# Kernel optimization log

Hardware: AMD Instinct MI355X
Metric: run time of the kernel (lower is better)

## Reference

```python
import jax, jax.numpy as jnp
import numpy as np

B, S, D, E, K = 4, 2048, 1024, 8, 2
DF = 4 * D


def setup_inputs() -> dict:
    key = jax.random.key(0)
    ks = jax.random.split(key, 7)
    x = jax.random.normal(ks[0], (B, S, D), dtype=jnp.float32)
    Wr = jax.random.normal(ks[1], (D, E), dtype=jnp.float32) * 0.02
    br = jnp.zeros((E,), dtype=jnp.float32)
    W1 = jax.random.normal(ks[2], (E, D, DF), dtype=jnp.float32) * 0.02
    b1 = jnp.zeros((E, DF), dtype=jnp.float32)
    W2 = jax.random.normal(ks[3], (E, DF, D), dtype=jnp.float32) * 0.02
    b2 = jnp.zeros((E, D), dtype=jnp.float32)
    return {"x": x, "Wr": Wr, "br": br, "W1": W1, "b1": b1, "W2": W2, "b2": b2}


def reference(x, Wr, br, W1, b1, W2, b2):
    # Router: softmax gates then top-k
    gates = jax.nn.softmax(x @ Wr + br, axis=-1)               # [B,S,E]
    topk_vals, topk_idx = jax.lax.top_k(gates, K)              # [B,S,K]

    # Per-(token, expert) combine weight: gate value if expert selected else 0
    onehot = jax.nn.one_hot(topk_idx, E, dtype=gates.dtype)    # [B,S,K,E]
    combine = jnp.sum(onehot * topk_vals[..., None], axis=2)   # [B,S,E]

    # Expert MLPs (loop over fixed small expert count, fully vectorized per expert)
    output = jnp.zeros_like(x)
    for e in range(E):
        h = jax.nn.gelu(x @ W1[e] + b1[e], approximate=False)  # [B,S,4D]
        y = h @ W2[e] + b2[e]                                  # [B,S,D]
        output = output + combine[..., e:e + 1] * y

    # Load-balancing aux loss (dispatch mask: 1.0 where expert selected)
    dispatch = jnp.max(onehot, axis=2)                         # [B,S,E]
    mean_gates = gates.mean(axis=(0, 1))
    mean_dispatch = dispatch.mean(axis=(0, 1))
    aux_loss = jnp.sum(mean_gates * mean_dispatch) * E / (B * S)
    return output, aux_loss
```

## Files before the change

### kernel.cpp

```cpp
#include <hip/hip_runtime.h>
#include <hip/hip_bf16.h>
#include <hip/hip_fp16.h>

typedef _Float16 f16;
typedef _Float16 half8 __attribute__((ext_vector_type(8)));
typedef _Float16 half4 __attribute__((ext_vector_type(4)));
typedef float   floatx4 __attribute__((ext_vector_type(4)));

#define N_TOK   8192
#define D_DIM   1024
#define E_NUM   8
#define DF_DIM  4096
#define MAX_SLOTS 17408
#define MAX_RT    136

#define MI_COUNT  0
#define MI_CURSOR 8
#define MI_OFF    16
#define MI_TOTAL  25
#define MI_RTE    26
#define MI_SUMG   168

__device__ __forceinline__ void gld_lds16(const void* g, void* l) {
    __builtin_amdgcn_global_load_lds(
        (__attribute__((address_space(1))) const void*)g,
        (__attribute__((address_space(3))) void*)l, 16, 0, 0);
}

__device__ __forceinline__ float gelu_f(float v) {
    float u = 0.7978845608028654f * v * (1.0f + 0.044715f * v * v);
    float t = __expf(-2.0f * fabsf(u));
    float th = (1.0f - t) / (1.0f + t);
    th = (u >= 0.f) ? th : -th;
    return 0.5f * v * (1.0f + th);
}

__global__ __launch_bounds__(256) void convert_x_kernel(
    const float* __restrict__ x, f16* __restrict__ xh)
{
    int idx = blockIdx.x * 256 + threadIdx.x;
    const int stride = gridDim.x * 256;
    const int n4 = (N_TOK * D_DIM) / 4;
    for (int i = idx; i < n4; i += stride) {
        float4 v = ((const float4*)x)[i];
        half4 o = { (f16)v.x, (f16)v.y, (f16)v.z, (f16)v.w };
        ((half4*)xh)[i] = o;
    }
}

__global__ __launch_bounds__(256) void transpose_conv_kernel(
    const float* __restrict__ src, f16* __restrict__ dst, int R, int C)
{
    const float* s = src + (size_t)blockIdx.z * R * C;
    f16* d = dst + (size_t)blockIdx.z * R * C;
    __shared__ float tile[64 * 65];
    const int rb = blockIdx.y * 64, cb = blockIdx.x * 64;
    const int tid = threadIdx.x;
#pragma unroll
    for (int j = 0; j < 4; ++j) {
        int lin = j * 1024 + tid * 4;
        int r = lin >> 6, c = lin & 63;
        float4 v = *(const float4*)(s + (size_t)(rb + r) * C + (cb + c));
        tile[r * 65 + c + 0] = v.x; tile[r * 65 + c + 1] = v.y;
        tile[r * 65 + c + 2] = v.z; tile[r * 65 + c + 3] = v.w;
    }
    __syncthreads();
#pragma unroll
    for (int j = 0; j < 4; ++j) {
        int lin = j * 1024 + tid * 4;
        int c = lin >> 6, r = lin & 63;
        half4 o = { (f16)tile[(r + 0) * 65 + c], (f16)tile[(r + 1) * 65 + c],
                    (f16)tile[(r + 2) * 65 + c], (f16)tile[(r + 3) * 65 + c] };
        *(half4*)(d + (size_t)(cb + c) * R + (rb + r)) = o;
    }
}

__global__ __launch_bounds__(256) void router_kernel(
    const float* __restrict__ x, const float* __restrict__ Wr,
    const float* __restrict__ br,
    int* __restrict__ topk_idx, float* __restrict__ topk_w,
    int* __restrict__ meta)
{
    const int w = threadIdx.x >> 6, l = threadIdx.x & 63;
    __shared__ float blk_sg[E_NUM];
    __shared__ int   blk_cnt[E_NUM];
    if (threadIdx.x < E_NUM) { blk_sg[threadIdx.x] = 0.f; blk_cnt[threadIdx.x] = 0; }
    __syncthreads();

    for (int it = 0; it < 4; ++it) {
        const int t = blockIdx.x * 16 + w * 4 + it;
        const float* xr = x + (size_t)t * D_DIM + l * 16;
        float acc[E_NUM] = {0.f,0.f,0.f,0.f,0.f,0.f,0.f,0.f};
#pragma unroll
        for (int i = 0; i < 16; i += 4) {
            float4 xv = *(const float4*)(xr + i);
            const float xs[4] = {xv.x, xv.y, xv.z, xv.w};
#pragma unroll
            for (int jj = 0; jj < 4; ++jj) {
                int d = l * 16 + i + jj;
                float4 w0 = *(const float4*)(Wr + (size_t)d * 8);
                float4 w1 = *(const float4*)(Wr + (size_t)d * 8 + 4);
                acc[0] += xs[jj] * w0.x; acc[1] += xs[jj] * w0.y;
                acc[2] += xs[jj] * w0.z; acc[3] += xs[jj] * w0.w;
                acc[4] += xs[jj] * w1.x; acc[5] += xs[jj] * w1.y;
                acc[6] += xs[jj] * w1.z; acc[7] += xs[jj] * w1.w;
            }
        }
#pragma unroll
        for (int e = 0; e < E_NUM; ++e) {
#pragma unroll
            for (int off = 32; off > 0; off >>= 1)
                acc[e] += __shfl_down(acc[e], off);
        }
        if (l == 0) {
            float lg[E_NUM], g[E_NUM];
            float mx = -1e30f;
#pragma unroll
            for (int e = 0; e < E_NUM; ++e) { lg[e] = acc[e] + br[e]; mx = fmaxf(mx, lg[e]); }
            float sum = 0.f;
#pragma unroll
            for (int e = 0; e < E_NUM; ++e) { g[e] = __expf(lg[e] - mx); sum += g[e]; }
            float inv = 1.f / sum;
#pragma unroll
            for (int e = 0; e < E_NUM; ++e) g[e] *= inv;
            int e1 = 0; float v1 = g[0];
#pragma unroll
            for (int e = 1; e < E_NUM; ++e) if (g[e] > v1) { v1 = g[e]; e1 = e; }
            int e2 = -1; float v2 = -1.f;
#pragma unroll
            for (int e = 0; e < E_NUM; ++e) if (e != e1 && g[e] > v2) { v2 = g[e]; e2 = e; }
            topk_idx[t * 2 + 0] = e1; topk_idx[t * 2 + 1] = e2;
            topk_w[t * 2 + 0] = v1;   topk_w[t * 2 + 1] = v2;
#pragma unroll
            for (int e = 0; e < E_NUM; ++e) atomicAdd(&blk_sg[e], g[e]);
            atomicAdd(&blk_cnt[e1], 1); atomicAdd(&blk_cnt[e2], 1);
        }
    }
    __syncthreads();
    if (threadIdx.x < E_NUM) {
        atomicAdd((float*)(meta + MI_SUMG) + threadIdx.x, blk_sg[threadIdx.x]);
        atomicAdd(meta + MI_COUNT + threadIdx.x, blk_cnt[threadIdx.x]);
    }
}

__global__ void scan_kernel(int* __restrict__ meta, float* __restrict__ out_aux)
{
    if (threadIdx.x != 0 || blockIdx.x != 0) return;
    int off = 0;
    for (int e = 0; e < E_NUM; ++e) {
        meta[MI_OFF + e] = off;
        int cnt = meta[MI_COUNT + e];
        int padded = ((cnt + 127) >> 7) << 7;
        for (int rt = off >> 7; rt < (off + padded) >> 7; ++rt)
            meta[MI_RTE + rt] = e;
        off += padded;
    }
    meta[MI_OFF + E_NUM] = off;
    meta[MI_TOTAL] = off >> 7;
    const float* sg = (const float*)(meta + MI_SUMG);
    float aux = 0.f;
    for (int e = 0; e < E_NUM; ++e)
        aux += (sg[e] / (float)N_TOK) * ((float)meta[MI_COUNT + e] / (float)N_TOK);
    out_aux[0] = aux * (float)E_NUM / (float)N_TOK;
}

__global__ __launch_bounds__(256) void fill_kernel(
    const int* __restrict__ topk_idx, const float* __restrict__ topk_w,
    int* __restrict__ meta, int* __restrict__ slot_token, float* __restrict__ slot_weight,
    int* __restrict__ slot_of)
{
    int t = blockIdx.x * 256 + threadIdx.x;
#pragma unroll
    for (int k = 0; k < 2; ++k) {
        int e = topk_idx[t * 2 + k];
        int p = atomicAdd(meta + MI_CURSOR + e, 1);
        int slot = meta[MI_OFF + e] + p;
        slot_token[slot] = t;
        slot_weight[slot] = topk_w[t * 2 + k];
        slot_of[t * 2 + k] = slot;
    }
}


#define STAGE_HALF(T, H) do {                                                  \
    f16* ld_ = smem + ((T)&1)*16384 + ((H)&1)*8192 + ((H)>>1)*4096;            \
    const f16* s_ = ((H)&1) ? bsrc[(H)>>1] : asrc[(H)>>1];                     \
    gld_lds16(s_ + (size_t)(T)*64, ld_ + tid*8);                               \
} while(0)

#define READ_AB() do {                                                         \
    _Pragma("unroll")                                                          \
    for (int mj = 0; mj < 4; ++mj) {                                           \
        const f16* pa_ = LA + (size_t)(rA + mj*16) * 64;                       \
        af[mj][0] = *(const half8*)(pa_ + sw0);                                \
        af[mj][1] = *(const half8*)(pa_ + sw1);                                \
    }                                                                          \
    _Pragma("unroll")                                                          \
    for (int nj = 0; nj < 2; ++nj) {                                           \
        const f16* pb_ = LB + (size_t)(rB + nj*16) * 64;                       \
        bf[nj][0] = *(const half8*)(pb_ + sw0);                                \
        bf[nj][1] = *(const half8*)(pb_ + sw1);                                \
    }                                                                          \
} while(0)

#define MFMA_MJ(MJ) do {                                                       \
    __builtin_amdgcn_s_setprio(1);                                             \
    _Pragma("unroll")                                                          \
    for (int nj = 0; nj < 2; ++nj) {                                           \
        acc[MJ][nj] = __builtin_amdgcn_mfma_f32_16x16x32_f16(                  \
            af[MJ][0], bf[nj][0], acc[MJ][nj], 0, 0, 0);                       \
        acc[MJ][nj] = __builtin_amdgcn_mfma_f32_16x16x32_f16(                  \
            af[MJ][1], bf[nj][1], acc[MJ][nj], 0, 0, 0);                       \
    }                                                                          \
    __builtin_amdgcn_s_setprio(0);                                             \
} while(0)

template<int KD, int NCOLS, int KSPLIT, bool GATHER, bool GELU, bool BIAS>
__global__ __launch_bounds__(512, 4) void gemm128_kernel(
    const f16* __restrict__ A, const f16* __restrict__ Bw,
    const float* __restrict__ bias, const int* __restrict__ slot_token,
    const int* __restrict__ meta, f16* __restrict__ Out, size_t out_kp_stride)
{
    constexpr int KLOC = KD / KSPLIT;
    constexpr int NT = KLOC / 64;
    __shared__ __align__(16) f16 smem[32768];

    const int rt = blockIdx.y;
    if (rt >= meta[MI_TOTAL]) return;
    const int e  = meta[MI_RTE + rt];
    const int nt = blockIdx.x;
    const int kp = blockIdx.z;
    const int kbase = kp * KLOC;

    const int tid = threadIdx.x;
    const int w = tid >> 6, l = tid & 63;
    const int wr2 = w >> 2, wc2 = w & 3;
    const int fr = l & 15, fq = l >> 4;

    const int srow = tid >> 3;
    const int kcs  = (tid & 7) ^ (srow & 7);

    const f16* asrc[2]; const f16* bsrc[2];
#pragma unroll
    for (int i = 0; i < 2; ++i) {
        int r = i * 64 + srow;
        int ar;
        if (GATHER) ar = slot_token[rt * 128 + r];
        else        ar = rt * 128 + r;
        asrc[i] = A + (size_t)ar * KD + kbase + kcs * 8;
        bsrc[i] = Bw + ((size_t)e * NCOLS + (size_t)nt * 128 + r) * KD + kbase + kcs * 8;
    }

    const int rA  = wr2 * 64 + fr;
    const int rB  = wc2 * 32 + fr;
    const int sw0 = ( fq      ^ (fr & 7)) * 8;
    const int sw1 = ((4 + fq) ^ (fr & 7)) * 8;

    floatx4 acc[4][2];
#pragma unroll
    for (int m = 0; m < 4; ++m)
#pragma unroll
        for (int n = 0; n < 2; ++n) acc[m][n] = (floatx4){0.f, 0.f, 0.f, 0.f};

    half8 af[4][2];
    half8 bf[2][2];

    STAGE_HALF(0, 0); STAGE_HALF(0, 1); STAGE_HALF(0, 2); STAGE_HALF(0, 3);
    STAGE_HALF(1, 0);
    asm volatile("s_waitcnt vmcnt(1)" ::: "memory");
    __builtin_amdgcn_s_barrier();

#pragma unroll 2
    for (int t = 0; t < NT; ++t) {
        const f16* LA = smem + (t & 1) * 16384;
        const f16* LB = LA + 8192;
        if (t + 1 < NT) { STAGE_HALF(t + 1, 1); STAGE_HALF(t + 1, 2); STAGE_HALF(t + 1, 3); }
        READ_AB();
        MFMA_MJ(0); MFMA_MJ(1); MFMA_MJ(2);
        asm volatile("s_waitcnt lgkmcnt(0)" ::: "memory");
        __builtin_amdgcn_s_barrier();
        if (t + 2 < NT) STAGE_HALF(t + 2, 0);
        MFMA_MJ(3);
        if (t + 1 < NT) {
            if (t + 1 < NT - 1) asm volatile("s_waitcnt vmcnt(1)" ::: "memory");
            else                asm volatile("s_waitcnt vmcnt(0)" ::: "memory");
            __builtin_amdgcn_s_barrier();
        }
    }

    f16* Op = Out + (size_t)kp * out_kp_stride;
    const int orow0 = rt * 128 + wr2 * 64;
    const int ocol0 = nt * 128 + wc2 * 32;
#pragma unroll
    for (int mj = 0; mj < 4; ++mj) {
#pragma unroll
        for (int nj = 0; nj < 2; ++nj) {
            const int col = ocol0 + nj * 16 + fr;
            float bs = 0.f;
            if (BIAS) bs = bias[(size_t)e * NCOLS + col];
#pragma unroll
            for (int j = 0; j < 4; ++j) {
                const int row = orow0 + mj * 16 + fq * 4 + j;
                float v = acc[mj][nj][j] + bs;
                if (GELU) v = gelu_f(v);
                Op[(size_t)row * NCOLS + col] = (f16)v;
            }
        }
    }
}

__global__ __launch_bounds__(256) void combine_kernel(
    const f16* __restrict__ P, const int* __restrict__ slot_of,
    const int* __restrict__ topk_idx, const float* __restrict__ topk_w,
    const float* __restrict__ b2, float* __restrict__ out)
{
    const int t = blockIdx.x;
    const int c = threadIdx.x;
    const size_t PS = (size_t)MAX_SLOTS * D_DIM;
    const int s0 = slot_of[t * 2], s1 = slot_of[t * 2 + 1];
    const int e0 = topk_idx[t * 2], e1 = topk_idx[t * 2 + 1];
    const float w0 = topk_w[t * 2], w1 = topk_w[t * 2 + 1];
    half4 a0 = *(const half4*)(P + (size_t)s0 * D_DIM + c * 4);
    half4 a1 = *(const half4*)(P + PS + (size_t)s0 * D_DIM + c * 4);
    half4 c0 = *(const half4*)(P + (size_t)s1 * D_DIM + c * 4);
    half4 c1 = *(const half4*)(P + PS + (size_t)s1 * D_DIM + c * 4);
    float4 bb0 = *(const float4*)(b2 + (size_t)e0 * D_DIM + c * 4);
    float4 bb1 = *(const float4*)(b2 + (size_t)e1 * D_DIM + c * 4);
    float4 o;
    o.x = w0 * ((float)a0[0] + (float)a1[0] + bb0.x) + w1 * ((float)c0[0] + (float)c1[0] + bb1.x);
    o.y = w0 * ((float)a0[1] + (float)a1[1] + bb0.y) + w1 * ((float)c0[1] + (float)c1[1] + bb1.y);
    o.z = w0 * ((float)a0[2] + (float)a1[2] + bb0.z) + w1 * ((float)c0[2] + (float)c1[2] + bb1.z);
    o.w = w0 * ((float)a0[3] + (float)a1[3] + bb0.w) + w1 * ((float)c0[3] + (float)c1[3] + bb1.w);
    *(float4*)(out + (size_t)t * D_DIM + c * 4) = o;
}

extern "C" void kernel_launch(void* const* d_in, const int* in_sizes, int n_in,
                              void* d_out, int out_size, void* d_ws, size_t ws_size,
                              hipStream_t stream) {
    const float* x  = (const float*)d_in[0];
    const float* Wr = (const float*)d_in[1];
    const float* br = (const float*)d_in[2];
    const float* W1 = (const float*)d_in[3];
    const float* b1 = (const float*)d_in[4];
    const float* W2 = (const float*)d_in[5];
    const float* b2 = (const float*)d_in[6];
    float* out = (float*)d_out;

    char* ws = (char*)d_ws;
    const size_t SZ_XH  = (size_t)N_TOK * D_DIM * 2;
    const size_t SZ_W1T = (size_t)E_NUM * DF_DIM * D_DIM * 2;
    const size_t SZ_W2T = SZ_W1T;
    const size_t SZ_H   = (size_t)MAX_SLOTS * DF_DIM * 2;

    f16* xh  = (f16*)(ws);
    f16* W1t = (f16*)(ws + SZ_XH);
    f16* W2t = (f16*)(ws + SZ_XH + SZ_W1T);
    f16* H   = (f16*)(ws + SZ_XH + SZ_W1T + SZ_W2T);
    f16* P   = (f16*)ws;
    char* p  = ws + SZ_XH + SZ_W1T + SZ_W2T + SZ_H;
    int*   topk_idx    = (int*)p;    p += (size_t)N_TOK * 2 * 4;
    float* topk_w      = (float*)p;  p += (size_t)N_TOK * 2 * 4;
    int*   slot_token  = (int*)p;    p += (size_t)MAX_SLOTS * 4;
    float* slot_weight = (float*)p;  p += (size_t)MAX_SLOTS * 4;
    int*   slot_of     = (int*)p;    p += (size_t)N_TOK * 2 * 4;
    int*   meta        = (int*)p;

    hipMemsetAsync(slot_token, 0, (size_t)MAX_SLOTS * 8 + (size_t)N_TOK * 2 * 4 + 1024, stream);

    convert_x_kernel<<<2048, 256, 0, stream>>>(x, xh);
    transpose_conv_kernel<<<dim3(DF_DIM / 64, D_DIM / 64, E_NUM), 256, 0, stream>>>(W1, W1t, D_DIM, DF_DIM);
    transpose_conv_kernel<<<dim3(D_DIM / 64, DF_DIM / 64, E_NUM), 256, 0, stream>>>(W2, W2t, DF_DIM, D_DIM);
    router_kernel<<<N_TOK / 16, 256, 0, stream>>>(x, Wr, br, topk_idx, topk_w, meta);
    scan_kernel<<<1, 64, 0, stream>>>(meta, out + (size_t)N_TOK * D_DIM);
    fill_kernel<<<N_TOK / 256, 256, 0, stream>>>(topk_idx, topk_w, meta, slot_token, slot_weight, slot_of);

    gemm128_kernel<D_DIM, DF_DIM, 1, true, true, true>
        <<<dim3(DF_DIM / 128, MAX_RT, 1), 512, 0, stream>>>(
        xh, W1t, b1, slot_token, meta, H, 0);

    gemm128_kernel<DF_DIM, D_DIM, 2, false, false, false>
        <<<dim3(D_DIM / 128, MAX_RT, 2), 512, 0, stream>>>(
        H, W2t, nullptr, slot_token, meta, P, (size_t)MAX_SLOTS * D_DIM);

    combine_kernel<<<N_TOK, 256, 0, stream>>>(P, slot_of, topk_idx, topk_w, b2, out);

    (void)in_sizes; (void)n_in; (void)ws_size;
}
```

Before: 635.7 us.

## Simplify GEMM to single-buffered 256-thread tiles with 64x64 per-wave output

Replaces the double-buffered, prefetching GEMM main loop with a single-buffered load-wait-compute loop using 256-thread blocks. Each wave now computes a 64x64 sub-tile with 16 accumulators, raising MFMA work per LDS read. The scan kernel fills the row-tile-to-expert table in parallel. In exchange, global-to-LDS loads no longer overlap with MFMA compute, and register pressure rises.

```diff
diff --git a/kernel.cpp b/kernel.cpp
--- a/kernel.cpp
+++ b/kernel.cpp
@@ -143,25 +143,35 @@
     }
 }
 
-__global__ void scan_kernel(int* __restrict__ meta, float* __restrict__ out_aux)
-{
-    if (threadIdx.x != 0 || blockIdx.x != 0) return;
-    int off = 0;
-    for (int e = 0; e < E_NUM; ++e) {
-        meta[MI_OFF + e] = off;
-        int cnt = meta[MI_COUNT + e];
-        int padded = ((cnt + 127) >> 7) << 7;
-        for (int rt = off >> 7; rt < (off + padded) >> 7; ++rt)
-            meta[MI_RTE + rt] = e;
-        off += padded;
-    }
-    meta[MI_OFF + E_NUM] = off;
-    meta[MI_TOTAL] = off >> 7;
-    const float* sg = (const float*)(meta + MI_SUMG);
-    float aux = 0.f;
-    for (int e = 0; e < E_NUM; ++e)
-        aux += (sg[e] / (float)N_TOK) * ((float)meta[MI_COUNT + e] / (float)N_TOK);
-    out_aux[0] = aux * (float)E_NUM / (float)N_TOK;
+__global__ __launch_bounds__(256) void scan_kernel(int* __restrict__ meta, float* __restrict__ out_aux)
+{
+    __shared__ int offs[E_NUM + 1];
+    const int tid = threadIdx.x;
+    if (tid == 0) {
+        int off = 0;
+        for (int e = 0; e < E_NUM; ++e) {
+            meta[MI_OFF + e] = off;
+            offs[e] = off;
+            int cnt = meta[MI_COUNT + e];
+            off += ((cnt + 127) >> 7) << 7;
+        }
+        meta[MI_OFF + E_NUM] = off;
+        offs[E_NUM] = off;
+        meta[MI_TOTAL] = off >> 7;
+        const float* sg = (const float*)(meta + MI_SUMG);
+        float aux = 0.f;
+        for (int e = 0; e < E_NUM; ++e)
+            aux += (sg[e] / (float)N_TOK) * ((float)meta[MI_COUNT + e] / (float)N_TOK);
+        out_aux[0] = aux * (float)E_NUM / (float)N_TOK;
+    }
+    __syncthreads();
+    const int total = offs[E_NUM] >> 7;
+    for (int rt = tid; rt < total; rt += 256) {
+        int row = rt << 7, e = 0;
+#pragma unroll
+        for (int k = 1; k < E_NUM; ++k) if (row >= offs[k]) e = k;
+        meta[MI_RTE + rt] = e;
+    }
 }
 
 __global__ __launch_bounds__(256) void fill_kernel(
@@ -182,48 +192,16 @@
 }
 
 
-#define STAGE_HALF(T, H) do {                                                  \
-    f16* ld_ = smem + ((T)&1)*16384 + ((H)&1)*8192 + ((H)>>1)*4096;            \
-    const f16* s_ = ((H)&1) ? bsrc[(H)>>1] : asrc[(H)>>1];                     \
-    gld_lds16(s_ + (size_t)(T)*64, ld_ + tid*8);                               \
-} while(0)
-
-#define READ_AB() do {                                                         \
-    _Pragma("unroll")                                                          \
-    for (int mj = 0; mj < 4; ++mj) {                                           \
-        const f16* pa_ = LA + (size_t)(rA + mj*16) * 64;                       \
-        af[mj][0] = *(const half8*)(pa_ + sw0);                                \
-        af[mj][1] = *(const half8*)(pa_ + sw1);                                \
-    }                                                                          \
-    _Pragma("unroll")                                                          \
-    for (int nj = 0; nj < 2; ++nj) {                                           \
-        const f16* pb_ = LB + (size_t)(rB + nj*16) * 64;                       \
-        bf[nj][0] = *(const half8*)(pb_ + sw0);                                \
-        bf[nj][1] = *(const half8*)(pb_ + sw1);                                \
-    }                                                                          \
-} while(0)
-
-#define MFMA_MJ(MJ) do {                                                       \
-    __builtin_amdgcn_s_setprio(1);                                             \
-    _Pragma("unroll")                                                          \
-    for (int nj = 0; nj < 2; ++nj) {                                           \
-        acc[MJ][nj] = __builtin_amdgcn_mfma_f32_16x16x32_f16(                  \
-            af[MJ][0], bf[nj][0], acc[MJ][nj], 0, 0, 0);                       \
-        acc[MJ][nj] = __builtin_amdgcn_mfma_f32_16x16x32_f16(                  \
-            af[MJ][1], bf[nj][1], acc[MJ][nj], 0, 0, 0);                       \
-    }                                                                          \
-    __builtin_amdgcn_s_setprio(0);                                             \
-} while(0)
-
 template<int KD, int NCOLS, int KSPLIT, bool GATHER, bool GELU, bool BIAS>
-__global__ __launch_bounds__(512, 4) void gemm128_kernel(
+__global__ __launch_bounds__(256, 3) void gemm128_kernel(
     const f16* __restrict__ A, const f16* __restrict__ Bw,
     const float* __restrict__ bias, const int* __restrict__ slot_token,
     const int* __restrict__ meta, f16* __restrict__ Out, size_t out_kp_stride)
 {
     constexpr int KLOC = KD / KSPLIT;
     constexpr int NT = KLOC / 64;
-    __shared__ __align__(16) f16 smem[32768];
+    __shared__ __align__(16) f16 As[128 * 64];
+    __shared__ __align__(16) f16 Bs[128 * 64];
 
     const int rt = blockIdx.y;
     if (rt >= meta[MI_TOTAL]) return;
@@ -234,16 +212,16 @@
 
     const int tid = threadIdx.x;
     const int w = tid >> 6, l = tid & 63;
-    const int wr2 = w >> 2, wc2 = w & 3;
+    const int wr2 = w >> 1, wc2 = w & 1;
     const int fr = l & 15, fq = l >> 4;
 
     const int srow = tid >> 3;
     const int kcs  = (tid & 7) ^ (srow & 7);
 
-    const f16* asrc[2]; const f16* bsrc[2];
-#pragma unroll
-    for (int i = 0; i < 2; ++i) {
-        int r = i * 64 + srow;
+    const f16* asrc[4]; const f16* bsrc[4];
+#pragma unroll
+    for (int i = 0; i < 4; ++i) {
+        int r = i * 32 + srow;
         int ar;
         if (GATHER) ar = slot_token[rt * 128 + r];
         else        ar = rt * 128 + r;
@@ -252,49 +230,53 @@
     }
 
     const int rA  = wr2 * 64 + fr;
-    const int rB  = wc2 * 32 + fr;
+    const int rB  = wc2 * 64 + fr;
     const int sw0 = ( fq      ^ (fr & 7)) * 8;
     const int sw1 = ((4 + fq) ^ (fr & 7)) * 8;
 
-    floatx4 acc[4][2];
+    floatx4 acc[4][4];
 #pragma unroll
     for (int m = 0; m < 4; ++m)
 #pragma unroll
-        for (int n = 0; n < 2; ++n) acc[m][n] = (floatx4){0.f, 0.f, 0.f, 0.f};
-
-    half8 af[4][2];
-    half8 bf[2][2];
-
-    STAGE_HALF(0, 0); STAGE_HALF(0, 1); STAGE_HALF(0, 2); STAGE_HALF(0, 3);
-    STAGE_HALF(1, 0);
-    asm volatile("s_waitcnt vmcnt(1)" ::: "memory");
-    __builtin_amdgcn_s_barrier();
+        for (int n = 0; n < 4; ++n) acc[m][n] = (floatx4){0.f, 0.f, 0.f, 0.f};
+
+    half8 af[4], bf[4];
 
 #pragma unroll 2
     for (int t = 0; t < NT; ++t) {
-        const f16* LA = smem + (t & 1) * 16384;
-        const f16* LB = LA + 8192;
-        if (t + 1 < NT) { STAGE_HALF(t + 1, 1); STAGE_HALF(t + 1, 2); STAGE_HALF(t + 1, 3); }
-        READ_AB();
-        MFMA_MJ(0); MFMA_MJ(1); MFMA_MJ(2);
-        asm volatile("s_waitcnt lgkmcnt(0)" ::: "memory");
+#pragma unroll
+        for (int i = 0; i < 4; ++i) {
+            gld_lds16(asrc[i] + (size_t)t * 64, &As[i * 2048 + tid * 8]);
+            gld_lds16(bsrc[i] + (size_t)t * 64, &Bs[i * 2048 + tid * 8]);
+        }
+        asm volatile("s_waitcnt vmcnt(0)" ::: "memory");
         __builtin_amdgcn_s_barrier();
-        if (t + 2 < NT) STAGE_HALF(t + 2, 0);
-        MFMA_MJ(3);
-        if (t + 1 < NT) {
-            if (t + 1 < NT - 1) asm volatile("s_waitcnt vmcnt(1)" ::: "memory");
-            else                asm volatile("s_waitcnt vmcnt(0)" ::: "memory");
-            __builtin_amdgcn_s_barrier();
-        }
+#pragma unroll
+        for (int kk2 = 0; kk2 < 2; ++kk2) {
+            const int sw = kk2 ? sw1 : sw0;
+#pragma unroll
+            for (int mj = 0; mj < 4; ++mj)
+                af[mj] = *(const half8*)&As[(size_t)(rA + mj * 16) * 64 + sw];
+#pragma unroll
+            for (int nj = 0; nj < 4; ++nj)
+                bf[nj] = *(const half8*)&Bs[(size_t)(rB + nj * 16) * 64 + sw];
+#pragma unroll
+            for (int mj = 0; mj < 4; ++mj)
+#pragma unroll
+                for (int nj = 0; nj < 4; ++nj)
+                    acc[mj][nj] = __builtin_amdgcn_mfma_f32_16x16x32_f16(
+                        af[mj], bf[nj], acc[mj][nj], 0, 0, 0);
+        }
+        __builtin_amdgcn_s_barrier();
     }
 
     f16* Op = Out + (size_t)kp * out_kp_stride;
     const int orow0 = rt * 128 + wr2 * 64;
-    const int ocol0 = nt * 128 + wc2 * 32;
+    const int ocol0 = nt * 128 + wc2 * 64;
 #pragma unroll
     for (int mj = 0; mj < 4; ++mj) {
 #pragma unroll
-        for (int nj = 0; nj < 2; ++nj) {
+        for (int nj = 0; nj < 4; ++nj) {
             const int col = ocol0 + nj * 16 + fr;
             float bs = 0.f;
             if (BIAS) bs = bias[(size_t)e * NCOLS + col];
@@ -371,15 +353,15 @@
     transpose_conv_kernel<<<dim3(DF_DIM / 64, D_DIM / 64, E_NUM), 256, 0, stream>>>(W1, W1t, D_DIM, DF_DIM);
     transpose_conv_kernel<<<dim3(D_DIM / 64, DF_DIM / 64, E_NUM), 256, 0, stream>>>(W2, W2t, DF_DIM, D_DIM);
     router_kernel<<<N_TOK / 16, 256, 0, stream>>>(x, Wr, br, topk_idx, topk_w, meta);
-    scan_kernel<<<1, 64, 0, stream>>>(meta, out + (size_t)N_TOK * D_DIM);
+    scan_kernel<<<1, 256, 0, stream>>>(meta, out + (size_t)N_TOK * D_DIM);
     fill_kernel<<<N_TOK / 256, 256, 0, stream>>>(topk_idx, topk_w, meta, slot_token, slot_weight, slot_of);
 
     gemm128_kernel<D_DIM, DF_DIM, 1, true, true, true>
-        <<<dim3(DF_DIM / 128, MAX_RT, 1), 512, 0, stream>>>(
+        <<<dim3(DF_DIM / 128, MAX_RT, 1), 256, 0, stream>>>(
         xh, W1t, b1, slot_token, meta, H, 0);
 
     gemm128_kernel<DF_DIM, D_DIM, 2, false, false, false>
-        <<<dim3(D_DIM / 128, MAX_RT, 2), 512, 0, stream>>>(
+        <<<dim3(D_DIM / 128, MAX_RT, 2), 256, 0, stream>>>(
         H, W2t, nullptr, slot_token, meta, P, (size_t)MAX_SLOTS * D_DIM);
 
     combine_kernel<<<N_TOK, 256, 0, stream>>>(P, slot_of, topk_idx, topk_w, b2, out);
```

New measurement: 585.6 us. 7.9% less time.
